# Optimization experiments

Measured on AMD Instinct MI355X. Metric: run time of the kernel, lower is better.

The kernel has to match this reference:

```python
import jax, jax.numpy as jnp
import numpy as np

N_FEATURES = 13
HIDDEN = 128


def setup_inputs() -> dict:
    key = jax.random.key(0)
    ks = jax.random.split(key, 7)
    F, H = N_FEATURES, HIDDEN
    # PyTorch LSTM init scale 1/sqrt(H)
    s = 1.0 / np.sqrt(H)
    return {
        "X": jax.random.normal(ks[0], (64, 32, 128, F), dtype=jnp.float32),
        "W_ih": jax.random.uniform(ks[1], (4 * H, F), minval=-s, maxval=s, dtype=jnp.float32),
        "W_hh": jax.random.uniform(ks[2], (4 * H, H), minval=-s, maxval=s, dtype=jnp.float32),
        "b_ih": jax.random.uniform(ks[3], (4 * H,), minval=-s, maxval=s, dtype=jnp.float32),
        "b_hh": jax.random.uniform(ks[4], (4 * H,), minval=-s, maxval=s, dtype=jnp.float32),
        "W_fc": jax.random.uniform(ks[5], (F, H), minval=-s, maxval=s, dtype=jnp.float32),
        "b_fc": jax.random.uniform(ks[6], (F,), minval=-s, maxval=s, dtype=jnp.float32),
    }


def _lstm_cell(x, h, c, W_ih, W_hh, b):
    # gates in PyTorch order: input, forget, cell(g), output
    gates = x @ W_ih.T + h @ W_hh.T + b  # (N, 4H)
    i, f, g, o = jnp.split(gates, 4, axis=-1)
    c_new = jax.nn.sigmoid(f) * c + jax.nn.sigmoid(i) * jnp.tanh(g)
    h_new = jax.nn.sigmoid(o) * jnp.tanh(c_new)
    return h_new, c_new


def reference(X, W_ih, W_hh, b_ih, b_hh, W_fc, b_fc):
    B, M, S, F = X.shape
    H = W_hh.shape[1]
    Xf = X.reshape(B * M, S, F)  # flatten (batch, blocks) -> N
    N = B * M
    b = b_ih + b_hh

    # ---- encoder: full-sequence LSTM, keep only final (h, c) ----
    def enc_step(carry, x_t):
        h, c = carry
        h, c = _lstm_cell(x_t, h, c, W_ih, W_hh, b)
        return (h, c), None

    h0 = jnp.zeros((N, H), X.dtype)
    (h_n, c_n), _ = jax.lax.scan(enc_step, (h0, h0), jnp.swapaxes(Xf, 0, 1))
    embeddings = h_n.reshape(B, M, H)

    def dec_step(carry, _):
        h, c, x = carry
        h, c = _lstm_cell(x, h, c, W_ih, W_hh, b)
        out = h @ W_fc.T + b_fc  # (N, F)
        return (h, c, out), out

    x0 = Xf[:, -1, :]  # last encoder input
    _, dec = jax.lax.scan(dec_step, (h_n, c_n, x0), None, length=S)  # (S, N, F)
    decoder_outputs = jnp.swapaxes(dec, 0, 1).reshape(B, M, S, F)
    return embeddings, decoder_outputs
```

## Files before the change

### kernel.cpp

```cpp
#include <hip/hip_runtime.h>

#define SEQS_PER_WG 8
#define HID 128
#define NF 13
#define SLEN 128
#define NSEQ 2048
#define ZSTRIDE 232

typedef _Float16 half8 __attribute__((ext_vector_type(8)));
typedef float floatx4 __attribute__((ext_vector_type(4)));

__device__ __forceinline__ float fast_rcp(float x) { return __builtin_amdgcn_rcpf(x); }
__device__ __forceinline__ float sigm(float x)  { return fast_rcp(1.0f + __expf(-x)); }
__device__ __forceinline__ float tanh_(float x) { return 1.0f - 2.0f * fast_rcp(1.0f + __expf(2.0f * x)); }

__device__ __forceinline__ float rowmerge(float a, float b) {
    auto pr = __builtin_amdgcn_permlane32_swap(__float_as_int(a), __float_as_int(b),
                                               false, false);
    return __int_as_float(pr[0]);
}

__global__ __launch_bounds__(256)
void weff_kernel(const float* __restrict__ W_ih, const float* __restrict__ W_hh,
                 const float* __restrict__ b_ih, const float* __restrict__ b_hh,
                 const float* __restrict__ W_fc, const float* __restrict__ b_fc,
                 _Float16* __restrict__ w_eff, float* __restrict__ b_eff)
{
    const int idx = blockIdx.x * 256 + threadIdx.x;
    const int n = idx >> 7, k = idx & 127;
    float s = W_hh[n * HID + k];
    #pragma unroll
    for (int f = 0; f < NF; ++f) s += W_ih[n * NF + f] * W_fc[f * HID + k];
    w_eff[n * HID + k] = (_Float16)s;
    if (k == 0) {
        float bb = b_ih[n] + b_hh[n];
        #pragma unroll
        for (int f = 0; f < NF; ++f) bb += W_ih[n * NF + f] * b_fc[f];
        b_eff[n] = bb;
    }
}

__global__ __launch_bounds__(512, 2)
void lstm_encdec_kernel(const float* __restrict__ X,
                        const float* __restrict__ W_ih,
                        const float* __restrict__ W_hh,
                        const float* __restrict__ b_ih,
                        const float* __restrict__ b_hh,
                        const float* __restrict__ W_fc,
                        const float* __restrict__ b_fc,
                        const _Float16* __restrict__ w_eff,
                        const float* __restrict__ b_eff,
                        float* __restrict__ out)
{
    __shared__ _Float16 zbuf[2][16 * ZSTRIDE];

    const int tid  = threadIdx.x;
    const int wave = tid >> 6;
    const int lane = tid & 63;
    const int quad = lane >> 4;
    const int lcol = lane & 15;
    const int row0 = (quad & 1) * 4 + ((quad >> 1) ? 2 : 0);
    const int unit = wave * 16 + lcol;
    const int seq0 = blockIdx.x * SEQS_PER_WG;

    half8 Bf[4][5];
    floatx4 biasv[4];
    #pragma unroll
    for (int g = 0; g < 4; ++g) {
        const int n = g * HID + unit;
        #pragma unroll
        for (int ks = 0; ks < 4; ++ks) {
            const float* p = W_hh + n * HID + ks * 32 + quad * 8;
            half8 v;
            #pragma unroll
            for (int j = 0; j < 8; ++j) v[j] = (_Float16)p[j];
            Bf[g][ks] = v;
        }
        {
            half8 v;
            #pragma unroll
            for (int j = 0; j < 8; ++j) {
                int kk = quad * 8 + j;
                v[j] = (kk < NF) ? (_Float16)W_ih[n * NF + kk] : (_Float16)0.0f;
            }
            Bf[g][4] = v;
        }
        float b = b_ih[n] + b_hh[n];
        biasv[g] = (floatx4){b, b, b, b};
    }

    half8 Wfcf[4];
    floatx4 bfcv = (floatx4){0.0f, 0.0f, 0.0f, 0.0f};
    if (wave == 0) {
        #pragma unroll
        for (int ks = 0; ks < 4; ++ks) {
            half8 v;
            #pragma unroll
            for (int j = 0; j < 8; ++j)
                v[j] = (lcol < NF) ? (_Float16)W_fc[lcol * HID + ks * 32 + quad * 8 + j]
                                   : (_Float16)0.0f;
            Wfcf[ks] = v;
        }
        float b = (lcol < NF) ? b_fc[lcol] : 0.0f;
        bfcv = (floatx4){b, b, b, b};
    }

    for (int i = tid; i < 2 * 16 * ZSTRIDE; i += 512)
        ((_Float16*)zbuf)[i] = (_Float16)0.0f;
    __syncthreads();

    const bool xact = tid < SEQS_PER_WG * NF;
    const int  xs = tid / NF, xf = tid % NF;
    const long xbase = (long)(seq0 + xs) * SLEN * NF + xf;
    if (xact) zbuf[0][xs * ZSTRIDE + HID + xf] = (_Float16)X[xbase];
    __syncthreads();

    float creg[2] = {0.0f, 0.0f};
    float h0 = 0.0f, h1 = 0.0f;
    int p = 0;

#define GATE_MFMA(NKS, ZR)                                                     \
    half8 a[5];                                                                \
    _Pragma("unroll")                                                          \
    for (int ks = 0; ks < (NKS); ++ks)                                         \
        a[ks] = *(const half8*)&(ZR)[lcol * ZSTRIDE + ks * 32 + quad * 8];     \
    floatx4 acc[4];                                                            \
    _Pragma("unroll")                                                          \
    for (int g = 0; g < 4; ++g)                                                \
        acc[g] = __builtin_amdgcn_mfma_f32_16x16x32_f16(a[0], Bf[g][0],        \
                                                        biasv[g], 0, 0, 0);    \
    _Pragma("unroll")                                                          \
    for (int ks = 1; ks < (NKS); ++ks)                                         \
        _Pragma("unroll")                                                      \
        for (int g = 0; g < 4; ++g)                                            \
            acc[g] = __builtin_amdgcn_mfma_f32_16x16x32_f16(a[ks], Bf[g][ks],  \
                                                            acc[g], 0, 0, 0);

#define GATES_EPILOGUE(ZW)                                                     \
    {                                                                          \
        float gv0[4], gv1[4];                                                  \
        _Pragma("unroll")                                                      \
        for (int g = 0; g < 4; ++g) {                                          \
            gv0[g] = rowmerge(acc[g][0], acc[g][2]);                           \
            gv1[g] = rowmerge(acc[g][1], acc[g][3]);                           \
        }                                                                      \
        float c0 = sigm(gv0[1]) * creg[0] + sigm(gv0[0]) * tanh_(gv0[2]);      \
        creg[0] = c0;                                                          \
        h0 = sigm(gv0[3]) * tanh_(c0);                                         \
        float c1 = sigm(gv1[1]) * creg[1] + sigm(gv1[0]) * tanh_(gv1[2]);      \
        creg[1] = c1;                                                          \
        h1 = sigm(gv1[3]) * tanh_(c1);                                         \
        (ZW)[(row0 + 0) * ZSTRIDE + unit] = (_Float16)h0;                      \
        (ZW)[(row0 + 1) * ZSTRIDE + unit] = (_Float16)h1;                      \
    }

    for (int t = 0; t < SLEN; ++t) {
        const int tn = (t + 1 < SLEN) ? t + 1 : SLEN - 1;
        float xpre = 0.0f;
        if (xact) xpre = X[xbase + tn * NF];

        const _Float16* zr = zbuf[p];
        _Float16* zw = zbuf[1 - p];

        GATE_MFMA(5, zr)
        GATES_EPILOGUE(zw)
        if (xact) zw[xs * ZSTRIDE + HID + xf] = (_Float16)xpre;

        __syncthreads();
        p ^= 1;
    }

    out[(long)(seq0 + row0 + 0) * HID + unit] = h0;
    out[(long)(seq0 + row0 + 1) * HID + unit] = h1;

    float* dec = out + (long)NSEQ * HID;

    {
        const _Float16* zr = zbuf[p];
        _Float16* zw = zbuf[1 - p];
        GATE_MFMA(5, zr)
        GATES_EPILOGUE(zw)
        __syncthreads();
        p ^= 1;
    }

    #pragma unroll
    for (int g = 0; g < 4; ++g) {
        const int n = g * HID + unit;
        #pragma unroll
        for (int ks = 0; ks < 4; ++ks)
            Bf[g][ks] = *(const half8*)&w_eff[n * HID + ks * 32 + quad * 8];
        const float bb = b_eff[n];
        biasv[g] = (floatx4){bb, bb, bb, bb};
    }

    for (int t = 1; t < SLEN; ++t) {
        const _Float16* zr = zbuf[p];
        _Float16* zw = zbuf[1 - p];

        GATE_MFMA(4, zr)

        if (wave == 0) {
            floatx4 o = bfcv;
            #pragma unroll
            for (int ks = 0; ks < 4; ++ks)
                o = __builtin_amdgcn_mfma_f32_16x16x32_f16(a[ks], Wfcf[ks], o, 0, 0, 0);
            if (quad < 2 && lcol < NF) {
                #pragma unroll
                for (int r = 0; r < 4; ++r)
                    dec[(long)(seq0 + quad * 4 + r) * SLEN * NF + (t - 1) * NF + lcol] = o[r];
            }
        }

        GATES_EPILOGUE(zw)

        __syncthreads();
        p ^= 1;
    }

    if (wave == 0) {
        const _Float16* zr = zbuf[p];
        half8 af[4];
        #pragma unroll
        for (int ks = 0; ks < 4; ++ks)
            af[ks] = *(const half8*)&zr[lcol * ZSTRIDE + ks * 32 + quad * 8];
        floatx4 o = bfcv;
        #pragma unroll
        for (int ks = 0; ks < 4; ++ks)
            o = __builtin_amdgcn_mfma_f32_16x16x32_f16(af[ks], Wfcf[ks], o, 0, 0, 0);
        if (quad < 2 && lcol < NF) {
            #pragma unroll
            for (int r = 0; r < 4; ++r)
                dec[(long)(seq0 + quad * 4 + r) * SLEN * NF + (SLEN - 1) * NF + lcol] = o[r];
        }
    }
}

extern "C" void kernel_launch(void* const* d_in, const int* in_sizes, int n_in,
                              void* d_out, int out_size, void* d_ws, size_t ws_size,
                              hipStream_t stream) {
    const float* X    = (const float*)d_in[0];
    const float* W_ih = (const float*)d_in[1];
    const float* W_hh = (const float*)d_in[2];
    const float* b_ih = (const float*)d_in[3];
    const float* b_hh = (const float*)d_in[4];
    const float* W_fc = (const float*)d_in[5];
    const float* b_fc = (const float*)d_in[6];
    float* out = (float*)d_out;

    _Float16* w_eff = (_Float16*)d_ws;
    float*    b_eff = (float*)((char*)d_ws + 4 * HID * HID * sizeof(_Float16));

    weff_kernel<<<(4 * HID * HID) / 256, 256, 0, stream>>>(
        W_ih, W_hh, b_ih, b_hh, W_fc, b_fc, w_eff, b_eff);

    lstm_encdec_kernel<<<NSEQ / SEQS_PER_WG, 512, 0, stream>>>(
        X, W_ih, W_hh, b_ih, b_hh, W_fc, b_fc, w_eff, b_eff, out);
}
```

Before: 280.0 us.

## Halve sequences per workgroup, use one MFMA row per lane, prescale weights for exp2

Result: slower. 404.0 us (+44.3%).

```diff
diff --git a/kernel.cpp b/kernel.cpp
--- a/kernel.cpp
+++ b/kernel.cpp
@@ -1,24 +1,20 @@
 #include <hip/hip_runtime.h>
 
-#define SEQS_PER_WG 8
+#define SEQS_PER_WG 4
 #define HID 128
 #define NF 13
 #define SLEN 128
 #define NSEQ 2048
 #define ZSTRIDE 232
+#define LOG2E 1.44269504088896340736f
 
 typedef _Float16 half8 __attribute__((ext_vector_type(8)));
 typedef float floatx4 __attribute__((ext_vector_type(4)));
 
 __device__ __forceinline__ float fast_rcp(float x) { return __builtin_amdgcn_rcpf(x); }
-__device__ __forceinline__ float sigm(float x)  { return fast_rcp(1.0f + __expf(-x)); }
-__device__ __forceinline__ float tanh_(float x) { return 1.0f - 2.0f * fast_rcp(1.0f + __expf(2.0f * x)); }
-
-__device__ __forceinline__ float rowmerge(float a, float b) {
-    auto pr = __builtin_amdgcn_permlane32_swap(__float_as_int(a), __float_as_int(b),
-                                               false, false);
-    return __int_as_float(pr[0]);
-}
+__device__ __forceinline__ float fast_ex2(float x) { return __builtin_amdgcn_exp2f(x); }
+__device__ __forceinline__ float sigm2(float x)  { return fast_rcp(1.0f + fast_ex2(-x)); }
+__device__ __forceinline__ float tanh2(float x)  { return 1.0f - 2.0f * fast_rcp(1.0f + fast_ex2(x)); }
 
 __global__ __launch_bounds__(256)
 void weff_kernel(const float* __restrict__ W_ih, const float* __restrict__ W_hh,
@@ -28,19 +24,20 @@
 {
     const int idx = blockIdx.x * 256 + threadIdx.x;
     const int n = idx >> 7, k = idx & 127;
+    const float sg = ((n >> 7) == 2) ? 2.0f * LOG2E : LOG2E;
     float s = W_hh[n * HID + k];
     #pragma unroll
     for (int f = 0; f < NF; ++f) s += W_ih[n * NF + f] * W_fc[f * HID + k];
-    w_eff[n * HID + k] = (_Float16)s;
+    w_eff[n * HID + k] = (_Float16)(s * sg);
     if (k == 0) {
         float bb = b_ih[n] + b_hh[n];
         #pragma unroll
         for (int f = 0; f < NF; ++f) bb += W_ih[n * NF + f] * b_fc[f];
-        b_eff[n] = bb;
+        b_eff[n] = bb * sg;
     }
 }
 
-__global__ __launch_bounds__(512, 2)
+__global__ __launch_bounds__(512, 4)
 void lstm_encdec_kernel(const float* __restrict__ X,
                         const float* __restrict__ W_ih,
                         const float* __restrict__ W_hh,
@@ -59,7 +56,6 @@
     const int lane = tid & 63;
     const int quad = lane >> 4;
     const int lcol = lane & 15;
-    const int row0 = (quad & 1) * 4 + ((quad >> 1) ? 2 : 0);
     const int unit = wave * 16 + lcol;
     const int seq0 = blockIdx.x * SEQS_PER_WG;
 
@@ -68,12 +64,13 @@
     #pragma unroll
     for (int g = 0; g < 4; ++g) {
         const int n = g * HID + unit;
+        const float sg = (g == 2) ? 2.0f * LOG2E : LOG2E;
         #pragma unroll
         for (int ks = 0; ks < 4; ++ks) {
             const float* p = W_hh + n * HID + ks * 32 + quad * 8;
             half8 v;
             #pragma unroll
-            for (int j = 0; j < 8; ++j) v[j] = (_Float16)p[j];
+            for (int j = 0; j < 8; ++j) v[j] = (_Float16)(p[j] * sg);
             Bf[g][ks] = v;
         }
         {
@@ -81,11 +78,11 @@
             #pragma unroll
             for (int j = 0; j < 8; ++j) {
                 int kk = quad * 8 + j;
-                v[j] = (kk < NF) ? (_Float16)W_ih[n * NF + kk] : (_Float16)0.0f;
+                v[j] = (kk < NF) ? (_Float16)(W_ih[n * NF + kk] * sg) : (_Float16)0.0f;
             }
             Bf[g][4] = v;
         }
-        float b = b_ih[n] + b_hh[n];
+        float b = (b_ih[n] + b_hh[n]) * sg;
         biasv[g] = (floatx4){b, b, b, b};
     }
 
@@ -112,11 +109,11 @@
     const bool xact = tid < SEQS_PER_WG * NF;
     const int  xs = tid / NF, xf = tid % NF;
     const long xbase = (long)(seq0 + xs) * SLEN * NF + xf;
-    if (xact) zbuf[0][xs * ZSTRIDE + HID + xf] = (_Float16)X[xbase];
+    if (xact) zbuf[0][4 * xs * ZSTRIDE + HID + xf] = (_Float16)X[xbase];
     __syncthreads();
 
-    float creg[2] = {0.0f, 0.0f};
-    float h0 = 0.0f, h1 = 0.0f;
+    float creg = 0.0f;
+    float hkeep = 0.0f;
     int p = 0;
 
 #define GATE_MFMA(NKS, ZR)                                                     \
@@ -138,20 +135,14 @@
 
 #define GATES_EPILOGUE(ZW)                                                     \
     {                                                                          \
-        float gv0[4], gv1[4];                                                  \
-        _Pragma("unroll")                                                      \
-        for (int g = 0; g < 4; ++g) {                                          \
-            gv0[g] = rowmerge(acc[g][0], acc[g][2]);                           \
-            gv1[g] = rowmerge(acc[g][1], acc[g][3]);                           \
-        }                                                                      \
-        float c0 = sigm(gv0[1]) * creg[0] + sigm(gv0[0]) * tanh_(gv0[2]);      \
-        creg[0] = c0;                                                          \
-        h0 = sigm(gv0[3]) * tanh_(c0);                                         \
-        float c1 = sigm(gv1[1]) * creg[1] + sigm(gv1[0]) * tanh_(gv1[2]);      \
-        creg[1] = c1;                                                          \
-        h1 = sigm(gv1[3]) * tanh_(c1);                                         \
-        (ZW)[(row0 + 0) * ZSTRIDE + unit] = (_Float16)h0;                      \
-        (ZW)[(row0 + 1) * ZSTRIDE + unit] = (_Float16)h1;                      \
+        float ii = sigm2(acc[0][0]);                                           \
+        float ff = sigm2(acc[1][0]);                                           \
+        float gg = tanh2(acc[2][0]);                                           \
+        float oo = sigm2(acc[3][0]);                                           \
+        float c  = ff * creg + ii * gg;                                        \
+        creg = c;                                                              \
+        hkeep = oo * tanh2(c * (2.0f * LOG2E));                                \
+        (ZW)[(4 * quad) * ZSTRIDE + unit] = (_Float16)hkeep;                   \
     }
 
     for (int t = 0; t < SLEN; ++t) {
@@ -164,14 +155,13 @@
 
         GATE_MFMA(5, zr)
         GATES_EPILOGUE(zw)
-        if (xact) zw[xs * ZSTRIDE + HID + xf] = (_Float16)xpre;
+        if (xact) zw[4 * xs * ZSTRIDE + HID + xf] = (_Float16)xpre;
 
         __syncthreads();
         p ^= 1;
     }
 
-    out[(long)(seq0 + row0 + 0) * HID + unit] = h0;
-    out[(long)(seq0 + row0 + 1) * HID + unit] = h1;
+    out[(long)(seq0 + quad) * HID + unit] = hkeep;
 
     float* dec = out + (long)NSEQ * HID;
 
@@ -205,11 +195,8 @@
             #pragma unroll
             for (int ks = 0; ks < 4; ++ks)
                 o = __builtin_amdgcn_mfma_f32_16x16x32_f16(a[ks], Wfcf[ks], o, 0, 0, 0);
-            if (quad < 2 && lcol < NF) {
-                #pragma unroll
-                for (int r = 0; r < 4; ++r)
-                    dec[(long)(seq0 + quad * 4 + r) * SLEN * NF + (t - 1) * NF + lcol] = o[r];
-            }
+            if (lcol < NF)
+                dec[(long)(seq0 + quad) * SLEN * NF + (t - 1) * NF + lcol] = o[0];
         }
 
         GATES_EPILOGUE(zw)
@@ -228,11 +215,8 @@
         #pragma unroll
         for (int ks = 0; ks < 4; ++ks)
             o = __builtin_amdgcn_mfma_f32_16x16x32_f16(af[ks], Wfcf[ks], o, 0, 0, 0);
-        if (quad < 2 && lcol < NF) {
-            #pragma unroll
-            for (int r = 0; r < 4; ++r)
-                dec[(long)(seq0 + quad * 4 + r) * SLEN * NF + (SLEN - 1) * NF + lcol] = o[r];
-        }
+        if (lcol < NF)
+            dec[(long)(seq0 + quad) * SLEN * NF + (SLEN - 1) * NF + lcol] = o[0];
     }
 }
 
```
